# Performance work log

Hardware: AMD Instinct MI355X
Metric: run time of the kernel (lower is better)

The kernel has to match this reference:

```python
import jax, jax.numpy as jnp
import numpy as np

B, T, CIN = 8, 1024, 6
D, L = 128, 2
DI, DS, DC, DTR = 256, 32, 4, 8  # d_inner=expand*d_model, d_state, d_conv, dt_rank=ceil(D/16)
BN_EPS = 1e-5


def setup_inputs() -> dict:
    key = jax.random.key(0)
    ks = jax.random.split(key, 8)
    s = 0.02
    A_log = jnp.log(jnp.broadcast_to(jnp.arange(1, DS + 1, dtype=jnp.float32), (L, DI, DS)))  # S4D-real init
    return {
        "x": jax.random.normal(ks[0], (B, T, CIN), jnp.float32),
        "conv_fw": jax.random.normal(ks[1], (D, CIN, 3), jnp.float32) * s,
        "conv_fb": jnp.zeros((D,), jnp.float32),
        "bn_g": jnp.ones((D,), jnp.float32),
        "bn_b": jnp.zeros((D,), jnp.float32),
        "rms_w": jnp.ones((L, D), jnp.float32),
        "W_in": jax.random.normal(ks[2], (L, D, 2 * DI), jnp.float32) * s,
        "conv_w": jax.random.normal(ks[3], (L, DI, DC), jnp.float32) * s,
        "conv_b": jnp.zeros((L, DI), jnp.float32),
        "W_xproj": jax.random.normal(ks[4], (L, DI, DTR + 2 * DS), jnp.float32) * s,
        "W_dt": jax.random.normal(ks[5], (L, DTR, DI), jnp.float32) * s,
        "b_dt": jnp.zeros((L, DI), jnp.float32),
        "A_log": A_log,
        "D_param": jnp.ones((L, DI), jnp.float32),
        "W_out": jax.random.normal(ks[6], (L, DI, D), jnp.float32) * s,
        "alpha": jnp.full((L,), 0.6, jnp.float32),
        "beta": jnp.full((L,), 0.99, jnp.float32),
        "norm_w": jnp.ones((D,), jnp.float32),
    }


def rmsnorm(x, w, eps=1e-6):
    return x * w * jax.lax.rsqrt(jnp.mean(x * x, axis=-1, keepdims=True) + eps)


def _mamba_block(x, rms_w, W_in, conv_w, conv_b, W_xproj, W_dt, b_dt, A_log, D_param, W_out, a, b):
    # pre-norm residual momentum-Mamba block; x: (B,T,D)
    xz = rmsnorm(x, rms_w) @ W_in            # (B,T,2*DI)
    xc, z = jnp.split(xz, 2, axis=-1)
    # depthwise causal conv over time
    xc = jnp.transpose(xc, (0, 2, 1))        # (B,DI,T)
    xc = jax.lax.conv_general_dilated(xc, conv_w[:, None, :], (1,), [(DC - 1, 0)],
                                      dimension_numbers=("NCH", "OIH", "NCH"), feature_group_count=DI)
    xc = jax.nn.silu(xc + conv_b[None, :, None])
    xc = jnp.transpose(xc, (0, 2, 1))        # (B,T,DI)
    xdbl = xc @ W_xproj                      # (B,T,DTR+2*DS)
    dtl, Bm, Cm = jnp.split(xdbl, [DTR, DTR + DS], axis=-1)
    dt = jax.nn.softplus(dtl @ W_dt + b_dt)  # (B,T,DI)
    A = -jnp.exp(A_log)                      # (DI,DS)
    dA = jnp.exp(dt[..., None] * A)          # (B,T,DI,DS)
    dBx = (dt * xc)[..., None] * Bm[:, :, None, :]  # (B,T,DI,DS)

    def step(carry, inp):
        h, v = carry
        dA_t, dBx_t, C_t = inp
        v = b * v + dBx_t                    # momentum accumulator (mode='real')
        h = dA_t * h + (1.0 - a) * dBx_t + a * v
        y = jnp.einsum("bds,bs->bd", h, C_t)
        return (h, v), y

    h0 = jnp.zeros((x.shape[0], DI, DS), x.dtype)
    _, ys = jax.lax.scan(step, (h0, h0),
                         (jnp.swapaxes(dA, 0, 1), jnp.swapaxes(dBx, 0, 1), jnp.swapaxes(Cm, 0, 1)))
    y = jnp.swapaxes(ys, 0, 1) + D_param * xc
    y = y * jax.nn.silu(z)
    return x + y @ W_out


def reference(x, conv_fw, conv_fb, bn_g, bn_b, rms_w, W_in, conv_w, conv_b, W_xproj,
              W_dt, b_dt, A_log, D_param, W_out, alpha, beta, norm_w):
    # frontend: Conv1d(k=3,pad=1) + BatchNorm1d(eval, running mean 0 var 1) + ReLU (dropout=identity in eval)
    h = jax.lax.conv_general_dilated(jnp.transpose(x, (0, 2, 1)), conv_fw, (1,), [(1, 1)],
                                     dimension_numbers=("NCH", "OIH", "NCH"))
    h = h + conv_fb[None, :, None]
    h = h * (bn_g / jnp.sqrt(1.0 + BN_EPS))[None, :, None] + bn_b[None, :, None]
    h = jax.nn.relu(h)
    h = jnp.transpose(h, (0, 2, 1))          # (B,T,D)
    for i in range(L):
        h = _mamba_block(h, rms_w[i], W_in[i], conv_w[i], conv_b[i], W_xproj[i], W_dt[i],
                         b_dt[i], A_log[i], D_param[i], W_out[i], alpha[i], beta[i])
    return rmsnorm(h, norm_w)
```

## Files before the change

kernel.cpp:

```cpp
#include <hip/hip_runtime.h>
#include <hip/hip_bf16.h>
#include <math.h>

constexpr int Bb  = 8;
constexpr int Tt  = 1024;
constexpr int CIN = 6;
constexpr int Dd  = 128;
constexpr int Ll  = 2;
constexpr int DI  = 256;
constexpr int DS  = 32;
constexpr int DC  = 4;
constexpr int DTR = 8;
constexpr int NX  = DTR + 2 * DS;
constexpr int ROWS = Bb * Tt;

using u16 = unsigned short;
using u32 = unsigned int;

typedef __attribute__((ext_vector_type(8))) short short8b;
typedef __attribute__((ext_vector_type(4))) float f32x4;

__device__ __forceinline__ float f4c(const float4& v, int k) {
  return k == 0 ? v.x : k == 1 ? v.y : k == 2 ? v.z : v.w;
}

__device__ __forceinline__ u16 f2bf(float f) {
  u32 x = __float_as_uint(f);
  u32 r = (x + 0x7fffu + ((x >> 16) & 1u)) >> 16;
  return (u16)r;
}
__device__ __forceinline__ u32 pack2bf(float lo, float hi) {
  return (u32)f2bf(lo) | ((u32)f2bf(hi) << 16);
}

template <int CTRL, int ROW_MASK>
__device__ __forceinline__ float dpp_add(float x) {
  int m = __builtin_amdgcn_update_dpp(0, __float_as_int(x), CTRL, ROW_MASK, 0xF, true);
  return x + __int_as_float(m);
}
__device__ __forceinline__ float half_wave_sum31(float p) {
  p = dpp_add<0x111, 0xF>(p);
  p = dpp_add<0x112, 0xF>(p);
  p = dpp_add<0x114, 0xF>(p);
  p = dpp_add<0x118, 0xF>(p);
  p = dpp_add<0x142, 0xA>(p);
  return p;
}

__global__ __launch_bounds__(128) void frontend_k(
    const float* __restrict__ x, const float* __restrict__ fw,
    const float* __restrict__ fb, const float* __restrict__ g,
    const float* __restrict__ bnb, float* __restrict__ h) {
  int t = blockIdx.x, b = blockIdx.y, d = threadIdx.x;
  float acc = 0.f;
#pragma unroll
  for (int k = 0; k < 3; ++k) {
    int tt = t - 1 + k;
    if (tt < 0 || tt >= Tt) continue;
    const float* xp = x + ((size_t)b * Tt + tt) * CIN;
#pragma unroll
    for (int c = 0; c < CIN; ++c)
      acc = fmaf(xp[c], fw[(d * CIN + c) * 3 + k], acc);
  }
  float scale = g[d] * rsqrtf(1.f + 1e-5f);
  float val = scale * (acc + fb[d]) + bnb[d];
  h[((size_t)b * Tt + t) * Dd + d] = fmaxf(val, 0.f);
}

__global__ __launch_bounds__(256) void rms_k(const float* __restrict__ in,
                                             const float* __restrict__ w,
                                             float* __restrict__ out) {
  int lane = threadIdx.x & 63;
  int row  = blockIdx.x * 4 + (threadIdx.x >> 6);
  const float* p = in + (size_t)row * Dd;
  float x0 = p[lane], x1 = p[lane + 64];
  float ss = fmaf(x0, x0, x1 * x1);
#pragma unroll
  for (int m = 1; m < 64; m <<= 1) ss += __shfl_xor(ss, m);
  float rs = rsqrtf(ss * (1.f / Dd) + 1e-6f);
  out[(size_t)row * Dd + lane]      = x0 * w[lane] * rs;
  out[(size_t)row * Dd + lane + 64] = x1 * w[lane + 64] * rs;
}

template <bool ADD_C>
__global__ __launch_bounds__(256) void sgemm_k(const float* __restrict__ A,
                                               const float* __restrict__ W,
                                               float* __restrict__ C,
                                               int M, int N, int K) {
  constexpr int BM = 128, BN = 64, BK = 32;
  __shared__ float As[BK][BM + 1];
  __shared__ float Ws[BK][BN];
  int tid = threadIdx.x;
  int tx = tid & 15, ty = tid >> 4;
  int bm = blockIdx.x * BM, bn = blockIdx.y * BN;
  float acc[8][4] = {};
  for (int k0 = 0; k0 < K; k0 += BK) {
#pragma unroll
    for (int i = 0; i < 4; ++i) {
      int qi = tid + i * 256;
      int r = qi >> 3, kq = (qi & 7) * 4;
      const float4 av = *(const float4*)(A + (size_t)(bm + r) * K + k0 + kq);
      As[kq + 0][r] = av.x; As[kq + 1][r] = av.y;
      As[kq + 2][r] = av.z; As[kq + 3][r] = av.w;
    }
#pragma unroll
    for (int i = 0; i < 2; ++i) {
      int qi = tid + i * 256;
      int kr = qi >> 4, nq = (qi & 15) * 4;
      int gn = bn + nq;
      float4 wv;
      if (gn + 3 < N) {
        wv = *(const float4*)(W + (size_t)(k0 + kr) * N + gn);
      } else {
        wv.x = (gn + 0 < N) ? W[(size_t)(k0 + kr) * N + gn + 0] : 0.f;
        wv.y = (gn + 1 < N) ? W[(size_t)(k0 + kr) * N + gn + 1] : 0.f;
        wv.z = (gn + 2 < N) ? W[(size_t)(k0 + kr) * N + gn + 2] : 0.f;
        wv.w = (gn + 3 < N) ? W[(size_t)(k0 + kr) * N + gn + 3] : 0.f;
      }
      *(float4*)&Ws[kr][nq] = wv;
    }
    __syncthreads();
#pragma unroll
    for (int kk = 0; kk < BK; ++kk) {
      float av[8], wv[4];
#pragma unroll
      for (int i = 0; i < 8; ++i) av[i] = As[kk][ty * 8 + i];
#pragma unroll
      for (int j = 0; j < 4; ++j) wv[j] = Ws[kk][tx * 4 + j];
#pragma unroll
      for (int i = 0; i < 8; ++i)
#pragma unroll
        for (int j = 0; j < 4; ++j)
          acc[i][j] = fmaf(av[i], wv[j], acc[i][j]);
    }
    __syncthreads();
  }
#pragma unroll
  for (int i = 0; i < 8; ++i) {
    int r = bm + ty * 8 + i;
#pragma unroll
    for (int j = 0; j < 4; ++j) {
      int c = bn + tx * 4 + j;
      if (c < N) {
        size_t off = (size_t)r * N + c;
        C[off] = acc[i][j] + (ADD_C ? C[off] : 0.f);
      }
    }
  }
}

__global__ __launch_bounds__(256) void wtrans_k(const float* __restrict__ W,
                                                u16* __restrict__ Wt,
                                                int K, int N) {
  __shared__ float tile[32][33];
  int k0 = blockIdx.x * 32, n0 = blockIdx.y * 32;
  int j = threadIdx.x & 31, i0 = threadIdx.x >> 5;
#pragma unroll
  for (int ii = 0; ii < 4; ++ii) {
    int k = i0 + ii * 8;
    tile[k][j] = W[(size_t)(k0 + k) * N + n0 + j];
  }
  __syncthreads();
  int kp = (threadIdx.x & 15) * 2;
  int nb = threadIdx.x >> 4;
#pragma unroll
  for (int half = 0; half < 2; ++half) {
    int n = nb + half * 16;
    u32 u = (u32)f2bf(tile[kp][n]) | ((u32)f2bf(tile[kp + 1][n]) << 16);
    *(u32*)&Wt[(size_t)(n0 + n) * K + k0 + kp] = u;
  }
}

template <bool ADD_C>
__global__ __launch_bounds__(256) void bgemm_k(
    const float* __restrict__ A, const u16* __restrict__ Wt,
    float* __restrict__ C, int M, int N, int K) {
  constexpr int BM = 128, BN = 64, BK = 32;
  constexpr int LDT = BK + 8;
  __shared__ u16 Al[BM][LDT];
  __shared__ u16 Wl[BN][LDT];
  int tid = threadIdx.x;
  int wid = tid >> 6, lane = tid & 63;
  int lrow = lane & 15, kh = lane >> 4;
  int bm = blockIdx.x * BM, bn = blockIdx.y * BN;

  f32x4 acc[2][4];
#pragma unroll
  for (int i = 0; i < 2; ++i)
#pragma unroll
    for (int j = 0; j < 4; ++j) acc[i][j] = (f32x4){0.f, 0.f, 0.f, 0.f};

  for (int k0 = 0; k0 < K; k0 += BK) {
    {
      int r = tid >> 1, hf = tid & 1;
      const float* ap = A + (size_t)(bm + r) * K + k0 + hf * 16;
      float4 a0 = *(const float4*)(ap + 0);
      float4 a1 = *(const float4*)(ap + 4);
      float4 a2 = *(const float4*)(ap + 8);
      float4 a3 = *(const float4*)(ap + 12);
      uint4 w0, w1;
      w0.x = pack2bf(a0.x, a0.y); w0.y = pack2bf(a0.z, a0.w);
      w0.z = pack2bf(a1.x, a1.y); w0.w = pack2bf(a1.z, a1.w);
      w1.x = pack2bf(a2.x, a2.y); w1.y = pack2bf(a2.z, a2.w);
      w1.z = pack2bf(a3.x, a3.y); w1.w = pack2bf(a3.z, a3.w);
      *(uint4*)&Al[r][hf * 16]     = w0;
      *(uint4*)&Al[r][hf * 16 + 8] = w1;
    }
    if (tid < 128) {
      int n = tid >> 1, hf = tid & 1;
      const uint4* wp = (const uint4*)(Wt + (size_t)(bn + n) * K + k0 + hf * 16);
      uint4 v0 = wp[0], v1 = wp[1];
      *(uint4*)&Wl[n][hf * 16]     = v0;
      *(uint4*)&Wl[n][hf * 16 + 8] = v1;
    }
    __syncthreads();

    short8b afr[2], wfr[4];
#pragma unroll
    for (int i = 0; i < 2; ++i)
      afr[i] = *(const short8b*)&Al[wid * 32 + i * 16 + lrow][kh * 8];
#pragma unroll
    for (int j = 0; j < 4; ++j)
      wfr[j] = *(const short8b*)&Wl[j * 16 + lrow][kh * 8];
#pragma unroll
    for (int i = 0; i < 2; ++i)
#pragma unroll
      for (int j = 0; j < 4; ++j)
        acc[i][j] = __builtin_amdgcn_mfma_f32_16x16x32_bf16(
            afr[i], wfr[j], acc[i][j], 0, 0, 0);
    __syncthreads();
  }

#pragma unroll
  for (int i = 0; i < 2; ++i) {
#pragma unroll
    for (int j = 0; j < 4; ++j) {
#pragma unroll
      for (int rg = 0; rg < 4; ++rg) {
        int row = bm + wid * 32 + i * 16 + kh * 4 + rg;
        int col = bn + j * 16 + lrow;
        size_t off = (size_t)row * N + col;
        C[off] = acc[i][j][rg] + (ADD_C ? C[off] : 0.f);
      }
    }
  }
}

__global__ __launch_bounds__(256) void convdw_k(const float* __restrict__ xz,
                                                const float* __restrict__ cw,
                                                const float* __restrict__ cb,
                                                float* __restrict__ xc) {
  int idx = blockIdx.x * 256 + threadIdx.x;
  int di = idx & (DI - 1);
  int bt = idx >> 8;
  int t  = bt & (Tt - 1);
  float s = cb[di];
#pragma unroll
  for (int k = 0; k < DC; ++k) {
    int tt = t - (DC - 1) + k;
    if (tt >= 0)
      s = fmaf(xz[(size_t)(bt - t + tt) * (2 * DI) + di], cw[di * DC + k], s);
  }
  xc[idx] = s / (1.f + expf(-s));
}

__global__ __launch_bounds__(256) void trans_k(
    const float* __restrict__ xdbl, const float* __restrict__ xc,
    const float* __restrict__ Wdt, const float* __restrict__ bdt,
    float* __restrict__ dtT, float* __restrict__ uT, float* __restrict__ bcT) {
  __shared__ float t1[32][33];
  __shared__ float t2[32][33];
  __shared__ float dtl[32][9];
  __shared__ float wts[8][33];
  __shared__ float bts[32];
  int t0 = blockIdx.x * 32, b = blockIdx.z, y = blockIdx.y;
  int tid = threadIdx.x;
  int j = tid & 31, i0 = tid >> 5;
  if (y < 8) {
    int di0 = y * 32;
    {
      int r = tid >> 3, c = tid & 7;
      dtl[r][c] = xdbl[((size_t)b * Tt + t0 + r) * NX + c];
      wts[i0][j] = Wdt[i0 * DI + di0 + j];
      if (tid < 32) bts[tid] = bdt[di0 + tid];
    }
    __syncthreads();
#pragma unroll
    for (int ii = 0; ii < 4; ++ii) {
      int i = i0 + ii * 8;
      float sacc = bts[j];
#pragma unroll
      for (int r = 0; r < 8; ++r) sacc = fmaf(dtl[i][r], wts[r][j], sacc);
      float sp = fmaxf(sacc, 0.f) + log1pf(expf(-fabsf(sacc)));
      float xcv = xc[((size_t)b * Tt + t0 + i) * DI + di0 + j];
      t1[i][j] = sp;
      t2[i][j] = sp * xcv;
    }
    __syncthreads();
#pragma unroll
    for (int ii = 0; ii < 4; ++ii) {
      int i = i0 + ii * 8;
      dtT[((size_t)b * DI + di0 + i) * Tt + t0 + j] = t1[j][i];
      uT [((size_t)b * DI + di0 + i) * Tt + t0 + j] = t2[j][i];
    }
  } else {
    int k0 = (y - 8) * 32;
#pragma unroll
    for (int ii = 0; ii < 4; ++ii) {
      int i = i0 + ii * 8;
      t1[i][j] = xdbl[((size_t)b * Tt + t0 + i) * NX + 8 + k0 + j];
    }
    __syncthreads();
#pragma unroll
    for (int ii = 0; ii < 4; ++ii) {
      int i = i0 + ii * 8;
      bcT[((size_t)b * 64 + k0 + i) * Tt + t0 + j] = t1[j][i];
    }
  }
}

__global__ __launch_bounds__(256) void scan2_k(
    const float* __restrict__ dtT, const float* __restrict__ uT,
    const float* __restrict__ bcT, const float* __restrict__ A_log,
    const float* __restrict__ alpha, const float* __restrict__ beta,
    float* __restrict__ pT, int layer) {
  int b = blockIdx.y;
  int hw = threadIdx.x >> 5, s = threadIdx.x & 31;
  int di = blockIdx.x * 8 + hw;
  float a = alpha[layer], bc = beta[layer], ab = a * bc;
  float Al2 = -expf(A_log[di * DS + s]) * 1.4426950408889634f;
  const float* dp = dtT + ((size_t)b * DI + di) * Tt;
  const float* up = uT  + ((size_t)b * DI + di) * Tt;
  const float* Bp = bcT + ((size_t)b * 64 + s) * Tt;
  const float* Cp = bcT + ((size_t)b * 64 + 32 + s) * Tt;
  float* pp = pT + ((size_t)b * DI + di) * Tt;

  float h = 0.f, v = 0.f;
  float4 dA_[4], uA_[4], BA_[4], CA_[4];
  float4 dB_[4], uB_[4], BB_[4], CB_[4];

  auto LOAD = [&](float4* d4, float4* u4, float4* B4, float4* C4, int c) {
    int t0 = c * 16;
#pragma unroll
    for (int q = 0; q < 4; ++q) {
      d4[q] = *(const float4*)(dp + t0 + q * 4);
      u4[q] = *(const float4*)(up + t0 + q * 4);
      B4[q] = *(const float4*)(Bp + t0 + q * 4);
      C4[q] = *(const float4*)(Cp + t0 + q * 4);
    }
  };
  auto COMP = [&](const float4* d4, const float4* u4, const float4* B4,
                  const float4* C4, int c) {
    int t0 = c * 16;
    float4 pv;
#pragma unroll
    for (int kk = 0; kk < 16; ++kk) {
      float dA  = exp2f(f4c(d4[kk >> 2], kk & 3) * Al2);
      float dBx = f4c(u4[kk >> 2], kk & 3) * f4c(B4[kk >> 2], kk & 3);
      float u2  = fmaf(ab, v, dBx);
      h = fmaf(dA, h, u2);
      v = fmaf(bc, v, dBx);
      float p = half_wave_sum31(h * f4c(C4[kk >> 2], kk & 3));
      if ((kk & 3) == 0) pv.x = p;
      else if ((kk & 3) == 1) pv.y = p;
      else if ((kk & 3) == 2) pv.z = p;
      else {
        pv.w = p;
        if (s == 31) *(float4*)(pp + t0 + (kk - 3)) = pv;
      }
    }
  };

  constexpr int NC = Tt / 16;
  LOAD(dA_, uA_, BA_, CA_, 0);
  for (int c = 0; c < NC; c += 2) {
    LOAD(dB_, uB_, BB_, CB_, c + 1);
    COMP(dA_, uA_, BA_, CA_, c);
    LOAD(dA_, uA_, BA_, CA_, (c + 2 < NC) ? c + 2 : NC - 1);
    COMP(dB_, uB_, BB_, CB_, c + 1);
  }
}

__global__ __launch_bounds__(256) void gate_k(
    const float* __restrict__ pT, const float* __restrict__ xc,
    const float* __restrict__ xz, const float* __restrict__ Dp_,
    float* __restrict__ y) {
  __shared__ float tile[32][33];
  int t0 = blockIdx.x * 32, di0 = blockIdx.y * 32, b = blockIdx.z;
  int j = threadIdx.x & 31, i0 = threadIdx.x >> 5;
#pragma unroll
  for (int ii = 0; ii < 4; ++ii) {
    int r = i0 + ii * 8;
    tile[r][j] = pT[((size_t)b * DI + di0 + r) * Tt + t0 + j];
  }
  __syncthreads();
#pragma unroll
  for (int ii = 0; ii < 4; ++ii) {
    int i = i0 + ii * 8;
    size_t row = (size_t)b * Tt + t0 + i;
    float p   = tile[j][i];
    float xcv = xc[row * DI + di0 + j];
    float zz  = xz[row * (2 * DI) + DI + di0 + j];
    float g   = zz / (1.f + expf(-zz));
    y[row * DI + di0 + j] = fmaf(Dp_[di0 + j], xcv, p) * g;
  }
}

extern "C" void kernel_launch(void* const* d_in, const int* in_sizes, int n_in,
                              void* d_out, int out_size, void* d_ws, size_t ws_size,
                              hipStream_t stream) {
  const float* x       = (const float*)d_in[0];
  const float* conv_fw = (const float*)d_in[1];
  const float* conv_fb = (const float*)d_in[2];
  const float* bn_g    = (const float*)d_in[3];
  const float* bn_b    = (const float*)d_in[4];
  const float* rms_w   = (const float*)d_in[5];
  const float* W_in    = (const float*)d_in[6];
  const float* conv_w  = (const float*)d_in[7];
  const float* conv_b  = (const float*)d_in[8];
  const float* W_xp    = (const float*)d_in[9];
  const float* W_dt    = (const float*)d_in[10];
  const float* b_dt    = (const float*)d_in[11];
  const float* A_log   = (const float*)d_in[12];
  const float* D_par   = (const float*)d_in[13];
  const float* W_out   = (const float*)d_in[14];
  const float* alpha   = (const float*)d_in[15];
  const float* beta    = (const float*)d_in[16];
  const float* norm_w  = (const float*)d_in[17];
  float* out = (float*)d_out;

  float* ws   = (float*)d_ws;
  float* h    = ws;
  float* xz   = h + 1048576;
  float* xc   = xz + 4194304;
  float* xdbl = xc + 2097152;
  float* pT   = xdbl + 589824;
  float* uT   = pT + 2097152;
  float* bcT  = uT + 2097152;
  float* shrd = bcT + 524288;
  u16*  wt_in  = (u16*)(shrd + 2097152);
  u16*  wt_out = wt_in + 2 * (2 * DI) * Dd;
  float* xn   = shrd;
  float* dtT  = shrd;
  float* ytot = shrd;

  for (int l = 0; l < Ll; ++l) {
    wtrans_k<<<dim3(Dd / 32, (2 * DI) / 32), 256, 0, stream>>>(
        W_in + (size_t)l * Dd * 2 * DI, wt_in + (size_t)l * (2 * DI) * Dd,
        Dd, 2 * DI);
    wtrans_k<<<dim3(DI / 32, Dd / 32), 256, 0, stream>>>(
        W_out + (size_t)l * DI * Dd, wt_out + (size_t)l * Dd * DI,
        DI, Dd);
  }

  frontend_k<<<dim3(Tt, Bb), 128, 0, stream>>>(x, conv_fw, conv_fb, bn_g, bn_b, h);

  for (int l = 0; l < Ll; ++l) {
    rms_k<<<ROWS / 4, 256, 0, stream>>>(h, rms_w + l * Dd, xn);
    bgemm_k<false><<<dim3(ROWS / 128, (2 * DI) / 64), 256, 0, stream>>>(
        xn, wt_in + (size_t)l * (2 * DI) * Dd, xz, ROWS, 2 * DI, Dd);
    convdw_k<<<(ROWS * DI) / 256, 256, 0, stream>>>(
        xz, conv_w + l * DI * DC, conv_b + l * DI, xc);
    sgemm_k<false><<<dim3(ROWS / 128, (NX + 63) / 64), 256, 0, stream>>>(
        xc, W_xp + (size_t)l * DI * NX, xdbl, ROWS, NX, DI);
    trans_k<<<dim3(Tt / 32, 10, Bb), 256, 0, stream>>>(
        xdbl, xc, W_dt + l * DTR * DI, b_dt + l * DI, dtT, uT, bcT);
    scan2_k<<<dim3(DI / 8, Bb), 256, 0, stream>>>(
        dtT, uT, bcT, A_log + l * DI * DS, alpha, beta, pT, l);
    gate_k<<<dim3(Tt / 32, DI / 32, Bb), 256, 0, stream>>>(
        pT, xc, xz, D_par + l * DI, ytot);
    bgemm_k<true><<<dim3(ROWS / 128, Dd / 64), 256, 0, stream>>>(
        ytot, wt_out + (size_t)l * Dd * DI, h, ROWS, Dd, DI);
  }

  rms_k<<<ROWS / 4, 256, 0, stream>>>(h, norm_w, out);
}
```

Before: 443.5 us.

## Fuse RMSNorm into in-projection GEMM, vectorize depthwise conv, batch weight transposes

Adds a bgemm_rms_k kernel that computes the RMSNorm scale per row, writes the normalized bf16 rows straight into shared memory and runs the full K=128 MFMA product from a single staged tile. This removes the separate rms_k launch and the xn round trip through global memory. The depthwise conv now handles four channels per thread with float4 loads and stores, the two weight-transpose launches per layer become one launch each over a z-grid dimension, and the scan buffers its 16 partial sums before writing. The fused kernel uses more LDS per block, which may reduce occupancy.

```diff
diff --git a/kernel.cpp b/kernel.cpp
--- a/kernel.cpp
+++ b/kernel.cpp
@@ -154,11 +154,14 @@
                                                 int K, int N) {
   __shared__ float tile[32][33];
   int k0 = blockIdx.x * 32, n0 = blockIdx.y * 32;
+  size_t lofs = (size_t)blockIdx.z * K * N;
+  const float* Wp = W + lofs;
+  u16* Wtp = Wt + lofs;
   int j = threadIdx.x & 31, i0 = threadIdx.x >> 5;
 #pragma unroll
   for (int ii = 0; ii < 4; ++ii) {
     int k = i0 + ii * 8;
-    tile[k][j] = W[(size_t)(k0 + k) * N + n0 + j];
+    tile[k][j] = Wp[(size_t)(k0 + k) * N + n0 + j];
   }
   __syncthreads();
   int kp = (threadIdx.x & 15) * 2;
@@ -167,8 +170,90 @@
   for (int half = 0; half < 2; ++half) {
     int n = nb + half * 16;
     u32 u = (u32)f2bf(tile[kp][n]) | ((u32)f2bf(tile[kp + 1][n]) << 16);
-    *(u32*)&Wt[(size_t)(n0 + n) * K + k0 + kp] = u;
-  }
+    *(u32*)&Wtp[(size_t)(n0 + n) * K + k0 + kp] = u;
+  }
+}
+
+__global__ __launch_bounds__(256) void bgemm_rms_k(
+    const float* __restrict__ A, const float* __restrict__ w,
+    const u16* __restrict__ Wt, float* __restrict__ C, int M, int N) {
+  constexpr int BM = 128, BN = 64, K = 128;
+  constexpr int LDT = K + 8;
+  __shared__ u16 Al[BM][LDT];
+  __shared__ u16 Wl[BN][LDT];
+  int tid = threadIdx.x;
+  int wid = tid >> 6, lane = tid & 63;
+  int lrow = lane & 15, kh = lane >> 4;
+  int bm = blockIdx.x * BM, bn = blockIdx.y * BN;
+
+  {
+    int r = tid >> 1, hf = tid & 1;
+    const float* ap = A + (size_t)(bm + r) * K + hf * 64;
+    float ss = 0.f;
+#pragma unroll
+    for (int q = 0; q < 16; ++q) {
+      float4 v = *(const float4*)(ap + q * 4);
+      ss += v.x * v.x + v.y * v.y + v.z * v.z + v.w * v.w;
+    }
+    ss += __shfl_xor(ss, 1);
+    float rs = rsqrtf(ss * (1.f / Dd) + 1e-6f);
+    const float* wp = w + hf * 64;
+#pragma unroll
+    for (int q = 0; q < 8; ++q) {
+      float4 v0 = *(const float4*)(ap + q * 8);
+      float4 v1 = *(const float4*)(ap + q * 8 + 4);
+      float4 w0 = *(const float4*)(wp + q * 8);
+      float4 w1 = *(const float4*)(wp + q * 8 + 4);
+      uint4 u;
+      u.x = pack2bf(v0.x * w0.x * rs, v0.y * w0.y * rs);
+      u.y = pack2bf(v0.z * w0.z * rs, v0.w * w0.w * rs);
+      u.z = pack2bf(v1.x * w1.x * rs, v1.y * w1.y * rs);
+      u.w = pack2bf(v1.z * w1.z * rs, v1.w * w1.w * rs);
+      *(uint4*)&Al[r][hf * 64 + q * 8] = u;
+    }
+  }
+  {
+    int n = tid >> 2, q = tid & 3;
+    const uint4* wp = (const uint4*)(Wt + (size_t)(bn + n) * K + q * 32);
+#pragma unroll
+    for (int i = 0; i < 4; ++i)
+      *(uint4*)&Wl[n][q * 32 + i * 8] = wp[i];
+  }
+  __syncthreads();
+
+  f32x4 acc[2][4];
+#pragma unroll
+  for (int i = 0; i < 2; ++i)
+#pragma unroll
+    for (int j = 0; j < 4; ++j) acc[i][j] = (f32x4){0.f, 0.f, 0.f, 0.f};
+
+#pragma unroll
+  for (int ks = 0; ks < 4; ++ks) {
+    short8b afr[2], wfr[4];
+#pragma unroll
+    for (int i = 0; i < 2; ++i)
+      afr[i] = *(const short8b*)&Al[wid * 32 + i * 16 + lrow][ks * 32 + kh * 8];
+#pragma unroll
+    for (int j = 0; j < 4; ++j)
+      wfr[j] = *(const short8b*)&Wl[j * 16 + lrow][ks * 32 + kh * 8];
+#pragma unroll
+    for (int i = 0; i < 2; ++i)
+#pragma unroll
+      for (int j = 0; j < 4; ++j)
+        acc[i][j] = __builtin_amdgcn_mfma_f32_16x16x32_bf16(
+            afr[i], wfr[j], acc[i][j], 0, 0, 0);
+  }
+
+#pragma unroll
+  for (int i = 0; i < 2; ++i)
+#pragma unroll
+    for (int j = 0; j < 4; ++j)
+#pragma unroll
+      for (int rg = 0; rg < 4; ++rg) {
+        int row = bm + wid * 32 + i * 16 + kh * 4 + rg;
+        int col = bn + j * 16 + lrow;
+        C[(size_t)row * N + col] = acc[i][j][rg];
+      }
 }
 
 template <bool ADD_C>
@@ -232,9 +317,9 @@
   }
 
 #pragma unroll
-  for (int i = 0; i < 2; ++i) {
-#pragma unroll
-    for (int j = 0; j < 4; ++j) {
+  for (int i = 0; i < 2; ++i)
+#pragma unroll
+    for (int j = 0; j < 4; ++j)
 #pragma unroll
       for (int rg = 0; rg < 4; ++rg) {
         int row = bm + wid * 32 + i * 16 + kh * 4 + rg;
@@ -242,26 +327,38 @@
         size_t off = (size_t)row * N + col;
         C[off] = acc[i][j][rg] + (ADD_C ? C[off] : 0.f);
       }
-    }
-  }
-}
-
-__global__ __launch_bounds__(256) void convdw_k(const float* __restrict__ xz,
-                                                const float* __restrict__ cw,
-                                                const float* __restrict__ cb,
-                                                float* __restrict__ xc) {
+}
+
+__global__ __launch_bounds__(256) void convdw4_k(const float* __restrict__ xz,
+                                                 const float* __restrict__ cw,
+                                                 const float* __restrict__ cb,
+                                                 float* __restrict__ xc) {
   int idx = blockIdx.x * 256 + threadIdx.x;
-  int di = idx & (DI - 1);
-  int bt = idx >> 8;
-  int t  = bt & (Tt - 1);
-  float s = cb[di];
+  int di4 = (idx & 63) * 4;
+  int bt  = idx >> 6;
+  int t   = bt & (Tt - 1);
+  float4 w0 = *(const float4*)&cw[(di4 + 0) * DC];
+  float4 w1 = *(const float4*)&cw[(di4 + 1) * DC];
+  float4 w2 = *(const float4*)&cw[(di4 + 2) * DC];
+  float4 w3 = *(const float4*)&cw[(di4 + 3) * DC];
+  float4 a = *(const float4*)&cb[di4];
 #pragma unroll
   for (int k = 0; k < DC; ++k) {
     int tt = t - (DC - 1) + k;
-    if (tt >= 0)
-      s = fmaf(xz[(size_t)(bt - t + tt) * (2 * DI) + di], cw[di * DC + k], s);
-  }
-  xc[idx] = s / (1.f + expf(-s));
+    if (tt >= 0) {
+      float4 v = *(const float4*)&xz[(size_t)(bt - t + tt) * (2 * DI) + di4];
+      a.x = fmaf(v.x, f4c(w0, k), a.x);
+      a.y = fmaf(v.y, f4c(w1, k), a.y);
+      a.z = fmaf(v.z, f4c(w2, k), a.z);
+      a.w = fmaf(v.w, f4c(w3, k), a.w);
+    }
+  }
+  float4 o;
+  o.x = a.x / (1.f + expf(-a.x));
+  o.y = a.y / (1.f + expf(-a.y));
+  o.z = a.z / (1.f + expf(-a.z));
+  o.w = a.w / (1.f + expf(-a.w));
+  *(float4*)&xc[(size_t)bt * DI + di4] = o;
 }
 
 __global__ __launch_bounds__(256) void trans_k(
@@ -352,7 +449,7 @@
   auto COMP = [&](const float4* d4, const float4* u4, const float4* B4,
                   const float4* C4, int c) {
     int t0 = c * 16;
-    float4 pv;
+    float pvs[16];
 #pragma unroll
     for (int kk = 0; kk < 16; ++kk) {
       float dA  = exp2f(f4c(d4[kk >> 2], kk & 3) * Al2);
@@ -360,13 +457,13 @@
       float u2  = fmaf(ab, v, dBx);
       h = fmaf(dA, h, u2);
       v = fmaf(bc, v, dBx);
-      float p = half_wave_sum31(h * f4c(C4[kk >> 2], kk & 3));
-      if ((kk & 3) == 0) pv.x = p;
-      else if ((kk & 3) == 1) pv.y = p;
-      else if ((kk & 3) == 2) pv.z = p;
-      else {
-        pv.w = p;
-        if (s == 31) *(float4*)(pp + t0 + (kk - 3)) = pv;
+      pvs[kk] = half_wave_sum31(h * f4c(C4[kk >> 2], kk & 3));
+    }
+    if (s == 31) {
+#pragma unroll
+      for (int q = 0; q < 4; ++q) {
+        float4 pv = {pvs[q * 4], pvs[q * 4 + 1], pvs[q * 4 + 2], pvs[q * 4 + 3]};
+        *(float4*)(pp + t0 + q * 4) = pv;
       }
     }
   };
@@ -440,26 +537,20 @@
   float* shrd = bcT + 524288;
   u16*  wt_in  = (u16*)(shrd + 2097152);
   u16*  wt_out = wt_in + 2 * (2 * DI) * Dd;
-  float* xn   = shrd;
   float* dtT  = shrd;
   float* ytot = shrd;
 
+  wtrans_k<<<dim3(Dd / 32, (2 * DI) / 32, Ll), 256, 0, stream>>>(
+      W_in, wt_in, Dd, 2 * DI);
+  wtrans_k<<<dim3(DI / 32, Dd / 32, Ll), 256, 0, stream>>>(
+      W_out, wt_out, DI, Dd);
+
+  frontend_k<<<dim3(Tt, Bb), 128, 0, stream>>>(x, conv_fw, conv_fb, bn_g, bn_b, h);
+
   for (int l = 0; l < Ll; ++l) {
-    wtrans_k<<<dim3(Dd / 32, (2 * DI) / 32), 256, 0, stream>>>(
-        W_in + (size_t)l * Dd * 2 * DI, wt_in + (size_t)l * (2 * DI) * Dd,
-        Dd, 2 * DI);
-    wtrans_k<<<dim3(DI / 32, Dd / 32), 256, 0, stream>>>(
-        W_out + (size_t)l * DI * Dd, wt_out + (size_t)l * Dd * DI,
-        DI, Dd);
-  }
-
-  frontend_k<<<dim3(Tt, Bb), 128, 0, stream>>>(x, conv_fw, conv_fb, bn_g, bn_b, h);
-
-  for (int l = 0; l < Ll; ++l) {
-    rms_k<<<ROWS / 4, 256, 0, stream>>>(h, rms_w + l * Dd, xn);
-    bgemm_k<false><<<dim3(ROWS / 128, (2 * DI) / 64), 256, 0, stream>>>(
-        xn, wt_in + (size_t)l * (2 * DI) * Dd, xz, ROWS, 2 * DI, Dd);
-    convdw_k<<<(ROWS * DI) / 256, 256, 0, stream>>>(
+    bgemm_rms_k<<<dim3(ROWS / 128, (2 * DI) / 64), 256, 0, stream>>>(
+        h, rms_w + l * Dd, wt_in + (size_t)l * (2 * DI) * Dd, xz, ROWS, 2 * DI);
+    convdw4_k<<<(ROWS * (DI / 4)) / 256, 256, 0, stream>>>(
         xz, conv_w + l * DI * DC, conv_b + l * DI, xc);
     sgemm_k<false><<<dim3(ROWS / 128, (NX + 63) / 64), 256, 0, stream>>>(
         xc, W_xp + (size_t)l * DI * NX, xdbl, ROWS, NX, DI);
```

Result: slower. 485.6 us (+9.5%).
